# Performance work log

Measured on AMD Instinct MI355X. Metric: run time of the kernel, lower is better.

Reference implementation:

```python
import jax, jax.numpy as jnp
import numpy as np

BN_EPS = 1e-5

def batch_norm(x, gamma, beta):
    # training-mode BatchNorm1d: biased batch stats over the edge dim
    mean = jnp.mean(x, axis=0)
    var = jnp.var(x, axis=0)
    return (x - mean) * jax.lax.rsqrt(var + BN_EPS) * gamma + beta

def setup_inputs() -> dict:
    key = jax.random.key(0)
    ks = jax.random.split(key, 10)
    N, F, E = 50000, 128, 600000
    D_in = 2 * F + 12  # 268
    h = jax.random.normal(ks[0], (N, F), dtype=jnp.float32)
    edge_feature = jax.random.normal(ks[1], (E, 12), dtype=jnp.float32)
    src = jax.random.randint(ks[2], (E,), 0, N)
    dst = jax.random.randint(ks[3], (E,), 0, N)
    def lin(k, fan_in, shape):
        bound = 1.0 / np.sqrt(fan_in)
        return jax.random.uniform(k, shape, jnp.float32, -bound, bound)
    W1 = lin(ks[4], D_in, (28, D_in)); b1 = lin(ks[5], D_in, (28,))
    W2 = lin(ks[6], 28, (8, 28));      b2 = lin(ks[7], 28, (8,))
    W3 = lin(ks[8], 8, (1, 8));        b3 = lin(ks[9], 8, (1,))
    gamma1 = jnp.ones((28,), jnp.float32); beta1 = jnp.zeros((28,), jnp.float32)
    gamma2 = jnp.ones((8,), jnp.float32);  beta2 = jnp.zeros((8,), jnp.float32)
    return {"h": h, "edge_feature": edge_feature, "src": src, "dst": dst,
            "W1": W1, "b1": b1, "gamma1": gamma1, "beta1": beta1,
            "W2": W2, "b2": b2, "gamma2": gamma2, "beta2": beta2,
            "W3": W3, "b3": b3}

def reference(h, edge_feature, src, dst, W1, b1, gamma1, beta1,
              W2, b2, gamma2, beta2, W3, b3):
    h_u = h[src]                    # [E, F] gather of source node feats
    h_v = h[dst]                    # [E, F] gather of dest node feats
    x = jnp.concatenate([h_u, h_v, edge_feature], axis=1)  # [E, 2F+12]
    s = jax.nn.relu(batch_norm(x @ W1.T + b1, gamma1, beta1))  # [E, 28]
    s = jax.nn.relu(batch_norm(s @ W2.T + b2, gamma2, beta2))  # [E, 8]
    score = s @ W3.T + b3           # [E, 1]
    return score
```

## Files before the change

### kernel.cpp

```cpp
#include <hip/hip_runtime.h>

#define BN_EPS 1e-5f


__global__ void k1_proj(const float* __restrict__ h, const float* __restrict__ W1,
                        float* __restrict__ P, float* __restrict__ stats, int N) {
  if (blockIdx.x == 0 && threadIdx.x < 72) stats[threadIdx.x] = 0.f;
  const int half = blockIdx.x & 1;
  const int node = (blockIdx.x >> 1) * 256 + threadIdx.x;
  if (node >= N) return;

  const float* __restrict__ wbase = W1 + half * 128;
  const float4* __restrict__ h4 = (const float4*)(h + (size_t)node * 128);

  float acc[28];
#pragma unroll
  for (int c = 0; c < 28; c++) acc[c] = 0.f;

  for (int kk = 0; kk < 16; kk++) {
    const float4 a = h4[kk * 2];
    const float4 b = h4[kk * 2 + 1];
#pragma unroll
    for (int c = 0; c < 28; c++) {
      const float* w = wbase + c * 268 + kk * 8;
      acc[c] += a.x * w[0] + a.y * w[1] + a.z * w[2] + a.w * w[3]
              + b.x * w[4] + b.y * w[5] + b.z * w[6] + b.w * w[7];
    }
  }

  float4* po = (float4*)(P + (size_t)node * 56 + half * 28);
#pragma unroll
  for (int q = 0; q < 7; q++) {
    po[q] = make_float4(acc[q * 4], acc[q * 4 + 1], acc[q * 4 + 2], acc[q * 4 + 3]);
  }
}

__global__ void k2_edge(const float* __restrict__ P, const float* __restrict__ ef,
                        const int* __restrict__ src, const int* __restrict__ dst,
                        const float* __restrict__ W1, const float* __restrict__ b1,
                        float* __restrict__ y1, float* __restrict__ stats, int E) {
  const int tid = threadIdx.x;
  const int c = tid & 31;
  const int g = tid >> 5;
  const bool act = (c < 28);
  float w[12];
  float bias = 0.f;
  if (act) {
    const float4* wp = (const float4*)(W1 + c * 268 + 256);
    float4 w0 = wp[0], w1 = wp[1], w2 = wp[2];
    w[0] = w0.x; w[1] = w0.y; w[2] = w0.z; w[3] = w0.w;
    w[4] = w1.x; w[5] = w1.y; w[6] = w1.z; w[7] = w1.w;
    w[8] = w2.x; w[9] = w2.y; w[10] = w2.z; w[11] = w2.w;
    bias = b1[c];
  }
  float sum = 0.f, ssq = 0.f;
  const int gstride = gridDim.x * 8;
  for (int e = blockIdx.x * 8 + g; e < E; e += gstride) {
    const int s = src[e], d = dst[e];
    if (act) {
      const float pa = P[s * 56 + c];
      const float pb = P[d * 56 + 28 + c];
      const float4* e4 = (const float4*)(ef + e * 12);
      float4 f0 = e4[0], f1 = e4[1], f2 = e4[2];
      float acc = bias
          + f0.x * w[0] + f0.y * w[1] + f0.z * w[2] + f0.w * w[3]
          + f1.x * w[4] + f1.y * w[5] + f1.z * w[6] + f1.w * w[7]
          + f2.x * w[8] + f2.y * w[9] + f2.z * w[10] + f2.w * w[11];
      const float v = acc + pa + pb;
      y1[e * 28 + c] = v;
      sum += v;
      ssq += v * v;
    }
  }
  sum += __shfl_xor(sum, 32);
  ssq += __shfl_xor(ssq, 32);
  __shared__ float red[2][4][28];
  const int wave = tid >> 6, lane = tid & 63;
  if (lane < 28) { red[0][wave][lane] = sum; red[1][wave][lane] = ssq; }
  __syncthreads();
  if (tid < 28) {
    atomicAdd(&stats[tid], red[0][0][tid] + red[0][1][tid] + red[0][2][tid] + red[0][3][tid]);
    atomicAdd(&stats[28 + tid], red[1][0][tid] + red[1][1][tid] + red[1][2][tid] + red[1][3][tid]);
  }
}

__global__ void k3_fin1(const float* __restrict__ gamma, const float* __restrict__ beta,
                        float* __restrict__ stats, float invE) {
  const int c = threadIdx.x;
  if (c < 28) {
    const float mean = stats[c] * invE;
    const float var = stats[28 + c] * invE - mean * mean;
    const float sc = gamma[c] * rsqrtf(var + BN_EPS);
    stats[72 + c] = sc;
    stats[100 + c] = beta[c] - mean * sc;
  }
}

__global__ void k4_l2(const float* __restrict__ y1, const float* __restrict__ stats,
                      const float* __restrict__ W2, const float* __restrict__ b2,
                      float* __restrict__ y2, float* __restrict__ stats2, int E) {
  float as[8], aq[8];
#pragma unroll
  for (int o = 0; o < 8; o++) { as[o] = 0.f; aq[o] = 0.f; }
  const int stride = gridDim.x * blockDim.x;
  for (int e = blockIdx.x * blockDim.x + threadIdx.x; e < E; e += stride) {
    const float4* p = (const float4*)(y1 + e * 28);
    float s1[28];
#pragma unroll
    for (int q = 0; q < 7; q++) {
      float4 v = p[q];
      s1[q * 4 + 0] = v.x; s1[q * 4 + 1] = v.y; s1[q * 4 + 2] = v.z; s1[q * 4 + 3] = v.w;
    }
    float acc[8];
#pragma unroll
    for (int o = 0; o < 8; o++) acc[o] = b2[o];
#pragma unroll
    for (int cc = 0; cc < 28; cc++) {
      float s = fmaxf(s1[cc] * stats[72 + cc] + stats[100 + cc], 0.f);
#pragma unroll
      for (int o = 0; o < 8; o++) acc[o] += W2[o * 28 + cc] * s;
    }
    float4* yo = (float4*)(y2 + e * 8);
    yo[0] = make_float4(acc[0], acc[1], acc[2], acc[3]);
    yo[1] = make_float4(acc[4], acc[5], acc[6], acc[7]);
#pragma unroll
    for (int o = 0; o < 8; o++) { as[o] += acc[o]; aq[o] += acc[o] * acc[o]; }
  }
#pragma unroll
  for (int o = 0; o < 8; o++) {
    for (int off = 32; off; off >>= 1) {
      as[o] += __shfl_down(as[o], off);
      aq[o] += __shfl_down(aq[o], off);
    }
  }
  __shared__ float redS[4][16];
  const int wave = threadIdx.x >> 6, lane = threadIdx.x & 63;
  if (lane == 0) {
#pragma unroll
    for (int o = 0; o < 8; o++) { redS[wave][o] = as[o]; redS[wave][8 + o] = aq[o]; }
  }
  __syncthreads();
  if (threadIdx.x < 16) {
    const int t = threadIdx.x;
    atomicAdd(&stats2[t], redS[0][t] + redS[1][t] + redS[2][t] + redS[3][t]);
  }
}

__global__ void k5_fin2(const float* __restrict__ gamma, const float* __restrict__ beta,
                        float* __restrict__ stats, float invE) {
  const int c = threadIdx.x;
  if (c < 8) {
    const float mean = stats[56 + c] * invE;
    const float var = stats[64 + c] * invE - mean * mean;
    const float sc = gamma[c] * rsqrtf(var + BN_EPS);
    stats[128 + c] = sc;
    stats[136 + c] = beta[c] - mean * sc;
  }
}

__global__ void k6_l3(const float* __restrict__ y2, const float* __restrict__ stats,
                      const float* __restrict__ W3, const float* __restrict__ b3,
                      float* __restrict__ out, int E) {
  const int e = blockIdx.x * blockDim.x + threadIdx.x;
  if (e >= E) return;
  const float4* p = (const float4*)(y2 + e * 8);
  float4 a = p[0], b4 = p[1];
  float v[8] = {a.x, a.y, a.z, a.w, b4.x, b4.y, b4.z, b4.w};
  float acc = b3[0];
#pragma unroll
  for (int o = 0; o < 8; o++) {
    float s = fmaxf(v[o] * stats[128 + o] + stats[136 + o], 0.f);
    acc += W3[o] * s;
  }
  out[e] = acc;
}

extern "C" void kernel_launch(void* const* d_in, const int* in_sizes, int n_in,
                              void* d_out, int out_size, void* d_ws, size_t ws_size,
                              hipStream_t stream) {
  const float* h   = (const float*)d_in[0];
  const float* ef  = (const float*)d_in[1];
  const int* src   = (const int*)d_in[2];
  const int* dst   = (const int*)d_in[3];
  const float* W1  = (const float*)d_in[4];
  const float* b1  = (const float*)d_in[5];
  const float* g1  = (const float*)d_in[6];
  const float* be1 = (const float*)d_in[7];
  const float* W2  = (const float*)d_in[8];
  const float* b2  = (const float*)d_in[9];
  const float* g2  = (const float*)d_in[10];
  const float* be2 = (const float*)d_in[11];
  const float* W3  = (const float*)d_in[12];
  const float* b3  = (const float*)d_in[13];
  float* out = (float*)d_out;

  const int N = in_sizes[0] / 128;
  const int E = in_sizes[2];
  const float invE = 1.0f / (float)E;

  float* ws = (float*)d_ws;
  float* stats = ws;
  float* P  = ws + 256;
  float* y1 = P + (size_t)N * 56;
  float* y2 = y1 + (size_t)E * 28;

  const int nodeBlocks = (N + 255) / 256;
  k1_proj<<<nodeBlocks * 2, 256, 0, stream>>>(h, W1, P, stats, N);
  k2_edge<<<1280, 256, 0, stream>>>(P, ef, src, dst, W1, b1, y1, stats, E);
  k3_fin1<<<1, 32, 0, stream>>>(g1, be1, stats, invE);
  k4_l2<<<1172, 256, 0, stream>>>(y1, stats, W2, b2, y2, stats + 56, E);
  k5_fin2<<<1, 64, 0, stream>>>(g2, be2, stats, invE);
  k6_l3<<<(E + 255) / 256, 256, 0, stream>>>(y2, stats, W3, b3, out, E);
}
```

Before: 287.0 us.

## Split node projections into padded src/dst tables, batch edges, fuse BN finalize

Stores the source and destination node projections in two separate tables padded to 32 floats per node, so each gather hits its own aligned row. The edge kernel now handles 4 edges per 32-lane group, using int4 index loads and contiguous edge-feature loads, and runs with more blocks and launch bounds. The two tiny BatchNorm finalize kernels are removed and folded into the last block of the preceding kernels through an atomic counter, which saves two launches. The Pdst table reuses the y2 buffer, which is only safe because k4 writes y2 after k2 has finished reading Pdst.

```diff
diff --git a/kernel.cpp b/kernel.cpp
--- a/kernel.cpp
+++ b/kernel.cpp
@@ -4,8 +4,12 @@
 
 
 __global__ void k1_proj(const float* __restrict__ h, const float* __restrict__ W1,
-                        float* __restrict__ P, float* __restrict__ stats, int N) {
-  if (blockIdx.x == 0 && threadIdx.x < 72) stats[threadIdx.x] = 0.f;
+                        float* __restrict__ Psrc, float* __restrict__ Pdst,
+                        float* __restrict__ stats, int N) {
+  if (blockIdx.x == 0) {
+    if (threadIdx.x < 72) stats[threadIdx.x] = 0.f;
+    if (threadIdx.x >= 144 && threadIdx.x < 146) stats[threadIdx.x] = 0.f;
+  }
   const int half = blockIdx.x & 1;
   const int node = (blockIdx.x >> 1) * 256 + threadIdx.x;
   if (node >= N) return;
@@ -28,22 +32,34 @@
     }
   }
 
-  float4* po = (float4*)(P + (size_t)node * 56 + half * 28);
+  float4* po = (float4*)((half ? Pdst : Psrc) + (size_t)node * 32);
 #pragma unroll
   for (int q = 0; q < 7; q++) {
     po[q] = make_float4(acc[q * 4], acc[q * 4 + 1], acc[q * 4 + 2], acc[q * 4 + 3]);
   }
-}
-
-__global__ void k2_edge(const float* __restrict__ P, const float* __restrict__ ef,
-                        const int* __restrict__ src, const int* __restrict__ dst,
-                        const float* __restrict__ W1, const float* __restrict__ b1,
-                        float* __restrict__ y1, float* __restrict__ stats, int E) {
+  po[7] = make_float4(0.f, 0.f, 0.f, 0.f);
+}
+
+#define DOT12(f0, f1, f2)                                               \
+  (f0.x * w[0] + f0.y * w[1] + f0.z * w[2] + f0.w * w[3]                \
+ + f1.x * w[4] + f1.y * w[5] + f1.z * w[6] + f1.w * w[7]                \
+ + f2.x * w[8] + f2.y * w[9] + f2.z * w[10] + f2.w * w[11])
+
+__global__ __launch_bounds__(256, 4)
+void k2_edge(const float* __restrict__ Psrc, const float* __restrict__ Pdst,
+             const float* __restrict__ ef,
+             const int* __restrict__ src, const int* __restrict__ dst,
+             const float* __restrict__ W1, const float* __restrict__ b1,
+             const float* __restrict__ g1, const float* __restrict__ be1,
+             float* __restrict__ y1, float* __restrict__ stats,
+             int E, float invE) {
   const int tid = threadIdx.x;
   const int c = tid & 31;
   const int g = tid >> 5;
   const bool act = (c < 28);
   float w[12];
+#pragma unroll
+  for (int k = 0; k < 12; k++) w[k] = 0.f;
   float bias = 0.f;
   if (act) {
     const float4* wp = (const float4*)(W1 + c * 268 + 256);
@@ -54,22 +70,50 @@
     bias = b1[c];
   }
   float sum = 0.f, ssq = 0.f;
-  const int gstride = gridDim.x * 8;
-  for (int e = blockIdx.x * 8 + g; e < E; e += gstride) {
-    const int s = src[e], d = dst[e];
-    if (act) {
-      const float pa = P[s * 56 + c];
-      const float pb = P[d * 56 + 28 + c];
-      const float4* e4 = (const float4*)(ef + e * 12);
-      float4 f0 = e4[0], f1 = e4[1], f2 = e4[2];
-      float acc = bias
-          + f0.x * w[0] + f0.y * w[1] + f0.z * w[2] + f0.w * w[3]
-          + f1.x * w[4] + f1.y * w[5] + f1.z * w[6] + f1.w * w[7]
-          + f2.x * w[8] + f2.y * w[9] + f2.z * w[10] + f2.w * w[11];
-      const float v = acc + pa + pb;
-      y1[e * 28 + c] = v;
-      sum += v;
-      ssq += v * v;
+  const int estride = gridDim.x * 32;
+  for (int base = (blockIdx.x * 8 + g) * 4; base < E; base += estride) {
+    if (base + 4 <= E) {
+      const int4 sv = *(const int4*)(src + base);
+      const int4 dv = *(const int4*)(dst + base);
+      const float pa0 = Psrc[(size_t)sv.x * 32 + c];
+      const float pa1 = Psrc[(size_t)sv.y * 32 + c];
+      const float pa2 = Psrc[(size_t)sv.z * 32 + c];
+      const float pa3 = Psrc[(size_t)sv.w * 32 + c];
+      const float pb0 = Pdst[(size_t)dv.x * 32 + c];
+      const float pb1 = Pdst[(size_t)dv.y * 32 + c];
+      const float pb2 = Pdst[(size_t)dv.z * 32 + c];
+      const float pb3 = Pdst[(size_t)dv.w * 32 + c];
+      const float4* e4 = (const float4*)(ef + (size_t)base * 12);
+      const float4 f00 = e4[0], f01 = e4[1], f02 = e4[2];
+      const float4 f10 = e4[3], f11 = e4[4], f12 = e4[5];
+      const float4 f20 = e4[6], f21 = e4[7], f22 = e4[8];
+      const float4 f30 = e4[9], f31 = e4[10], f32 = e4[11];
+      const float v0 = bias + DOT12(f00, f01, f02) + pa0 + pb0;
+      const float v1 = bias + DOT12(f10, f11, f12) + pa1 + pb1;
+      const float v2 = bias + DOT12(f20, f21, f22) + pa2 + pb2;
+      const float v3 = bias + DOT12(f30, f31, f32) + pa3 + pb3;
+      if (act) {
+        y1[(size_t)(base + 0) * 28 + c] = v0;
+        y1[(size_t)(base + 1) * 28 + c] = v1;
+        y1[(size_t)(base + 2) * 28 + c] = v2;
+        y1[(size_t)(base + 3) * 28 + c] = v3;
+      }
+      sum += (v0 + v1) + (v2 + v3);
+      ssq += (v0 * v0 + v1 * v1) + (v2 * v2 + v3 * v3);
+    } else {
+      for (int i = 0; i < 4; i++) {
+        const int e = base + i;
+        if (e >= E) break;
+        const int s = src[e], d = dst[e];
+        const float pa = Psrc[(size_t)s * 32 + c];
+        const float pb = Pdst[(size_t)d * 32 + c];
+        const float4* e4 = (const float4*)(ef + (size_t)e * 12);
+        const float4 f0 = e4[0], f1 = e4[1], f2 = e4[2];
+        const float v = bias + DOT12(f0, f1, f2) + pa + pb;
+        if (act) y1[(size_t)e * 28 + c] = v;
+        sum += v;
+        ssq += v * v;
+      }
     }
   }
   sum += __shfl_xor(sum, 32);
@@ -82,29 +126,34 @@
     atomicAdd(&stats[tid], red[0][0][tid] + red[0][1][tid] + red[0][2][tid] + red[0][3][tid]);
     atomicAdd(&stats[28 + tid], red[1][0][tid] + red[1][1][tid] + red[1][2][tid] + red[1][3][tid]);
   }
-}
-
-__global__ void k3_fin1(const float* __restrict__ gamma, const float* __restrict__ beta,
-                        float* __restrict__ stats, float invE) {
-  const int c = threadIdx.x;
-  if (c < 28) {
-    const float mean = stats[c] * invE;
-    const float var = stats[28 + c] * invE - mean * mean;
-    const float sc = gamma[c] * rsqrtf(var + BN_EPS);
-    stats[72 + c] = sc;
-    stats[100 + c] = beta[c] - mean * sc;
-  }
-}
-
-__global__ void k4_l2(const float* __restrict__ y1, const float* __restrict__ stats,
+  __syncthreads();
+  __shared__ int lastFlag;
+  if (tid == 0) {
+    __threadfence();
+    lastFlag = (atomicAdd((int*)(stats + 144), 1) == (int)gridDim.x - 1);
+  }
+  __syncthreads();
+  if (lastFlag && tid < 28) {
+    const float s = atomicAdd(&stats[tid], 0.f);
+    const float q = atomicAdd(&stats[28 + tid], 0.f);
+    const float mean = s * invE;
+    const float var = q * invE - mean * mean;
+    const float sc = g1[tid] * rsqrtf(var + BN_EPS);
+    stats[72 + tid] = sc;
+    stats[100 + tid] = be1[tid] - mean * sc;
+  }
+}
+
+__global__ void k4_l2(const float* __restrict__ y1, float* __restrict__ stats,
                       const float* __restrict__ W2, const float* __restrict__ b2,
-                      float* __restrict__ y2, float* __restrict__ stats2, int E) {
+                      const float* __restrict__ g2, const float* __restrict__ be2,
+                      float* __restrict__ y2, int E, float invE) {
   float as[8], aq[8];
 #pragma unroll
   for (int o = 0; o < 8; o++) { as[o] = 0.f; aq[o] = 0.f; }
   const int stride = gridDim.x * blockDim.x;
   for (int e = blockIdx.x * blockDim.x + threadIdx.x; e < E; e += stride) {
-    const float4* p = (const float4*)(y1 + e * 28);
+    const float4* p = (const float4*)(y1 + (size_t)e * 28);
     float s1[28];
 #pragma unroll
     for (int q = 0; q < 7; q++) {
@@ -120,7 +169,7 @@
 #pragma unroll
       for (int o = 0; o < 8; o++) acc[o] += W2[o * 28 + cc] * s;
     }
-    float4* yo = (float4*)(y2 + e * 8);
+    float4* yo = (float4*)(y2 + (size_t)e * 8);
     yo[0] = make_float4(acc[0], acc[1], acc[2], acc[3]);
     yo[1] = make_float4(acc[4], acc[5], acc[6], acc[7]);
 #pragma unroll
@@ -142,19 +191,24 @@
   __syncthreads();
   if (threadIdx.x < 16) {
     const int t = threadIdx.x;
-    atomicAdd(&stats2[t], redS[0][t] + redS[1][t] + redS[2][t] + redS[3][t]);
-  }
-}
-
-__global__ void k5_fin2(const float* __restrict__ gamma, const float* __restrict__ beta,
-                        float* __restrict__ stats, float invE) {
-  const int c = threadIdx.x;
-  if (c < 8) {
-    const float mean = stats[56 + c] * invE;
-    const float var = stats[64 + c] * invE - mean * mean;
-    const float sc = gamma[c] * rsqrtf(var + BN_EPS);
-    stats[128 + c] = sc;
-    stats[136 + c] = beta[c] - mean * sc;
+    atomicAdd(&stats[56 + t], redS[0][t] + redS[1][t] + redS[2][t] + redS[3][t]);
+  }
+  __syncthreads();
+  __shared__ int lastFlag;
+  if (threadIdx.x == 0) {
+    __threadfence();
+    lastFlag = (atomicAdd((int*)(stats + 145), 1) == (int)gridDim.x - 1);
+  }
+  __syncthreads();
+  if (lastFlag && threadIdx.x < 8) {
+    const int t = threadIdx.x;
+    const float s = atomicAdd(&stats[56 + t], 0.f);
+    const float q = atomicAdd(&stats[64 + t], 0.f);
+    const float mean = s * invE;
+    const float var = q * invE - mean * mean;
+    const float sc = g2[t] * rsqrtf(var + BN_EPS);
+    stats[128 + t] = sc;
+    stats[136 + t] = be2[t] - mean * sc;
   }
 }
 
@@ -163,7 +217,7 @@
                       float* __restrict__ out, int E) {
   const int e = blockIdx.x * blockDim.x + threadIdx.x;
   if (e >= E) return;
-  const float4* p = (const float4*)(y2 + e * 8);
+  const float4* p = (const float4*)(y2 + (size_t)e * 8);
   float4 a = p[0], b4 = p[1];
   float v[8] = {a.x, a.y, a.z, a.w, b4.x, b4.y, b4.z, b4.w};
   float acc = b3[0];
@@ -200,15 +254,14 @@
 
   float* ws = (float*)d_ws;
   float* stats = ws;
-  float* P  = ws + 256;
-  float* y1 = P + (size_t)N * 56;
+  float* Psrc = ws + 256;
+  float* y1 = Psrc + (size_t)N * 32;
   float* y2 = y1 + (size_t)E * 28;
+  float* Pdst = y2;
 
   const int nodeBlocks = (N + 255) / 256;
-  k1_proj<<<nodeBlocks * 2, 256, 0, stream>>>(h, W1, P, stats, N);
-  k2_edge<<<1280, 256, 0, stream>>>(P, ef, src, dst, W1, b1, y1, stats, E);
-  k3_fin1<<<1, 32, 0, stream>>>(g1, be1, stats, invE);
-  k4_l2<<<1172, 256, 0, stream>>>(y1, stats, W2, b2, y2, stats + 56, E);
-  k5_fin2<<<1, 64, 0, stream>>>(g2, be2, stats, invE);
+  k1_proj<<<nodeBlocks * 2, 256, 0, stream>>>(h, W1, Psrc, Pdst, stats, N);
+  k2_edge<<<2048, 256, 0, stream>>>(Psrc, Pdst, ef, src, dst, W1, b1, g1, be1, y1, stats, E, invE);
+  k4_l2<<<1172, 256, 0, stream>>>(y1, stats, W2, b2, g2, be2, y2, E, invE);
   k6_l3<<<(E + 255) / 256, 256, 0, stream>>>(y2, stats, W3, b3, out, E);
 }
```

Result: slower. 373.5 us (+30.1%).

## Split node projections into padded src/dst arrays and stage layer-2 input through LDS

Applied to the files above, without the earlier changes.

The node projection buffer is split into separate src and dst arrays, each padded to 32 floats per node. This aligns the per-edge gathers to 128-byte rows, and the dst array reuses the y2 workspace region. The layer-2 kernel now loads each 256-edge tile of y1 with coalesced float4 reads into padded shared memory instead of doing strided per-thread row loads, and it launches one block per tile. This adds two barriers per tile and a large LDS allocation that may limit occupancy.

```diff
diff --git a/kernel.cpp b/kernel.cpp
--- a/kernel.cpp
+++ b/kernel.cpp
@@ -4,7 +4,8 @@
 
 
 __global__ void k1_proj(const float* __restrict__ h, const float* __restrict__ W1,
-                        float* __restrict__ P, float* __restrict__ stats, int N) {
+                        float* __restrict__ Psrc, float* __restrict__ Pdst,
+                        float* __restrict__ stats, int N) {
   if (blockIdx.x == 0 && threadIdx.x < 72) stats[threadIdx.x] = 0.f;
   const int half = blockIdx.x & 1;
   const int node = (blockIdx.x >> 1) * 256 + threadIdx.x;
@@ -28,14 +29,16 @@
     }
   }
 
-  float4* po = (float4*)(P + (size_t)node * 56 + half * 28);
+  float4* po = (float4*)((half ? Pdst : Psrc) + (size_t)node * 32);
 #pragma unroll
   for (int q = 0; q < 7; q++) {
     po[q] = make_float4(acc[q * 4], acc[q * 4 + 1], acc[q * 4 + 2], acc[q * 4 + 3]);
   }
-}
-
-__global__ void k2_edge(const float* __restrict__ P, const float* __restrict__ ef,
+  po[7] = make_float4(0.f, 0.f, 0.f, 0.f);
+}
+
+__global__ void k2_edge(const float* __restrict__ Psrc, const float* __restrict__ Pdst,
+                        const float* __restrict__ ef,
                         const int* __restrict__ src, const int* __restrict__ dst,
                         const float* __restrict__ W1, const float* __restrict__ b1,
                         float* __restrict__ y1, float* __restrict__ stats, int E) {
@@ -58,16 +61,16 @@
   for (int e = blockIdx.x * 8 + g; e < E; e += gstride) {
     const int s = src[e], d = dst[e];
     if (act) {
-      const float pa = P[s * 56 + c];
-      const float pb = P[d * 56 + 28 + c];
-      const float4* e4 = (const float4*)(ef + e * 12);
+      const float pa = Psrc[(size_t)s * 32 + c];
+      const float pb = Pdst[(size_t)d * 32 + c];
+      const float4* e4 = (const float4*)(ef + (size_t)e * 12);
       float4 f0 = e4[0], f1 = e4[1], f2 = e4[2];
       float acc = bias
           + f0.x * w[0] + f0.y * w[1] + f0.z * w[2] + f0.w * w[3]
           + f1.x * w[4] + f1.y * w[5] + f1.z * w[6] + f1.w * w[7]
           + f2.x * w[8] + f2.y * w[9] + f2.z * w[10] + f2.w * w[11];
       const float v = acc + pa + pb;
-      y1[e * 28 + c] = v;
+      y1[(size_t)e * 28 + c] = v;
       sum += v;
       ssq += v * v;
     }
@@ -96,36 +99,46 @@
   }
 }
 
-__global__ void k4_l2(const float* __restrict__ y1, const float* __restrict__ stats,
+__global__ void k4_l2(const float* __restrict__ y1, const float* __restrict__ statsRO,
                       const float* __restrict__ W2, const float* __restrict__ b2,
-                      float* __restrict__ y2, float* __restrict__ stats2, int E) {
+                      float* __restrict__ y2, float* __restrict__ statsW, int E) {
+  __shared__ float tile[256 * 29];
   float as[8], aq[8];
 #pragma unroll
   for (int o = 0; o < 8; o++) { as[o] = 0.f; aq[o] = 0.f; }
-  const int stride = gridDim.x * blockDim.x;
-  for (int e = blockIdx.x * blockDim.x + threadIdx.x; e < E; e += stride) {
-    const float4* p = (const float4*)(y1 + e * 28);
-    float s1[28];
-#pragma unroll
-    for (int q = 0; q < 7; q++) {
-      float4 v = p[q];
-      s1[q * 4 + 0] = v.x; s1[q * 4 + 1] = v.y; s1[q * 4 + 2] = v.z; s1[q * 4 + 3] = v.w;
-    }
-    float acc[8];
-#pragma unroll
-    for (int o = 0; o < 8; o++) acc[o] = b2[o];
-#pragma unroll
-    for (int cc = 0; cc < 28; cc++) {
-      float s = fmaxf(s1[cc] * stats[72 + cc] + stats[100 + cc], 0.f);
-#pragma unroll
-      for (int o = 0; o < 8; o++) acc[o] += W2[o * 28 + cc] * s;
-    }
-    float4* yo = (float4*)(y2 + e * 8);
-    yo[0] = make_float4(acc[0], acc[1], acc[2], acc[3]);
-    yo[1] = make_float4(acc[4], acc[5], acc[6], acc[7]);
-#pragma unroll
-    for (int o = 0; o < 8; o++) { as[o] += acc[o]; aq[o] += acc[o] * acc[o]; }
-  }
+
+  for (int tileBase = blockIdx.x * 256; tileBase < E; tileBase += gridDim.x * 256) {
+    const int nEdge = min(256, E - tileBase);
+    const int total = nEdge * 28;
+    const float* gp = y1 + (size_t)tileBase * 28;
+    for (int j = threadIdx.x * 4; j < total; j += 1024) {
+      const float4 v = *(const float4*)(gp + j);
+      const int e = j / 28;
+      const int cc = j - e * 28;
+      float* lr = &tile[e * 29 + cc];
+      lr[0] = v.x; lr[1] = v.y; lr[2] = v.z; lr[3] = v.w;
+    }
+    __syncthreads();
+    if ((int)threadIdx.x < nEdge) {
+      const float* s1 = &tile[threadIdx.x * 29];
+      float acc[8];
+#pragma unroll
+      for (int o = 0; o < 8; o++) acc[o] = b2[o];
+#pragma unroll
+      for (int cc = 0; cc < 28; cc++) {
+        const float s = fmaxf(s1[cc] * statsRO[72 + cc] + statsRO[100 + cc], 0.f);
+#pragma unroll
+        for (int o = 0; o < 8; o++) acc[o] += W2[o * 28 + cc] * s;
+      }
+      float4* yo = (float4*)(y2 + (size_t)(tileBase + threadIdx.x) * 8);
+      yo[0] = make_float4(acc[0], acc[1], acc[2], acc[3]);
+      yo[1] = make_float4(acc[4], acc[5], acc[6], acc[7]);
+#pragma unroll
+      for (int o = 0; o < 8; o++) { as[o] += acc[o]; aq[o] += acc[o] * acc[o]; }
+    }
+    __syncthreads();
+  }
+
 #pragma unroll
   for (int o = 0; o < 8; o++) {
     for (int off = 32; off; off >>= 1) {
@@ -142,7 +155,7 @@
   __syncthreads();
   if (threadIdx.x < 16) {
     const int t = threadIdx.x;
-    atomicAdd(&stats2[t], redS[0][t] + redS[1][t] + redS[2][t] + redS[3][t]);
+    atomicAdd(&statsW[56 + t], redS[0][t] + redS[1][t] + redS[2][t] + redS[3][t]);
   }
 }
 
@@ -163,7 +176,7 @@
                       float* __restrict__ out, int E) {
   const int e = blockIdx.x * blockDim.x + threadIdx.x;
   if (e >= E) return;
-  const float4* p = (const float4*)(y2 + e * 8);
+  const float4* p = (const float4*)(y2 + (size_t)e * 8);
   float4 a = p[0], b4 = p[1];
   float v[8] = {a.x, a.y, a.z, a.w, b4.x, b4.y, b4.z, b4.w};
   float acc = b3[0];
@@ -200,15 +213,17 @@
 
   float* ws = (float*)d_ws;
   float* stats = ws;
-  float* P  = ws + 256;
-  float* y1 = P + (size_t)N * 56;
+  float* Psrc = ws + 256;
+  float* y1 = Psrc + (size_t)N * 32;
   float* y2 = y1 + (size_t)E * 28;
+  float* Pdst = y2;
 
   const int nodeBlocks = (N + 255) / 256;
-  k1_proj<<<nodeBlocks * 2, 256, 0, stream>>>(h, W1, P, stats, N);
-  k2_edge<<<1280, 256, 0, stream>>>(P, ef, src, dst, W1, b1, y1, stats, E);
+  const int nTiles = (E + 255) / 256;
+  k1_proj<<<nodeBlocks * 2, 256, 0, stream>>>(h, W1, Psrc, Pdst, stats, N);
+  k2_edge<<<1280, 256, 0, stream>>>(Psrc, Pdst, ef, src, dst, W1, b1, y1, stats, E);
   k3_fin1<<<1, 32, 0, stream>>>(g1, be1, stats, invE);
-  k4_l2<<<1172, 256, 0, stream>>>(y1, stats, W2, b2, y2, stats + 56, E);
+  k4_l2<<<nTiles, 256, 0, stream>>>(y1, stats, W2, b2, y2, stats, E);
   k5_fin2<<<1, 64, 0, stream>>>(g2, be2, stats, invE);
-  k6_l3<<<(E + 255) / 256, 256, 0, stream>>>(y2, stats, W3, b3, out, E);
-}
+  k6_l3<<<nTiles, 256, 0, stream>>>(y2, stats, W3, b3, out, E);
+}
```

New measurement: 298.4 us. +4.0%, slower.
